# Kernel tuning notes

Measured on AMD Instinct MI355X. Metric: run time of the kernel, lower is better.

Reference implementation:

```python
import jax, jax.numpy as jnp
import numpy as np

N = 8192          # number of samples (atoms)
D_IN = 256        # in_features (descriptor dim)
D_OUT = 256       # out_features
NUM_TYPE = 64     # number of atom types
INIT_VAL = 0.01


def setup_inputs() -> dict:
    key = jax.random.key(0)
    k1, k2, k3, k4 = jax.random.split(key, 4)
    batch_i = jax.random.randint(k1, (N,), 0, NUM_TYPE)                     # [N] type index per sample
    batch_descriptor = jax.random.normal(k2, (N, D_IN), dtype=jnp.float32)  # [N, D_IN]
    layer1 = INIT_VAL * jax.random.normal(k3, (NUM_TYPE, D_OUT, D_IN), dtype=jnp.float32)
    W = INIT_VAL * jax.random.normal(k4, (D_OUT, D_IN), dtype=jnp.float32)  # linear_adjust.weight
    b = jnp.zeros((D_OUT,), dtype=jnp.float32)                              # linear_adjust.bias (init 0)
    return {"batch_i": batch_i, "batch_descriptor": batch_descriptor,
            "layer1": layer1, "W": W, "b": b}


def reference(batch_i, batch_descriptor, layer1, W, b):
    # Per-sample type-indexed weight gather + batched mat-vec (torch.bmm)
    # layer1[batch_i]: [N, D_OUT, D_IN]; descriptor: [N, D_IN] -> [N, D_OUT]
    gathered = layer1[batch_i]
    out = jnp.einsum('noi,ni->no', gathered, batch_descriptor)
    out = jnp.tanh(out)  # ACT assumed tanh (undefined in snippet)
    # linear_adjust: x @ W.T + b
    adjust = batch_descriptor @ W.T + b
    return out + adjust
```

## Files before the change

### kernel.cpp

```cpp
#include <hip/hip_runtime.h>
#include <cstddef>

#define NUM_TYPE 64
#define DD 256
#define NN 8192
#define PSTR 264
#define PT 512

typedef __bf16 bf16x8 __attribute__((ext_vector_type(8)));
typedef __bf16 bf16x4 __attribute__((ext_vector_type(4)));
typedef float f32x4 __attribute__((ext_vector_type(4)));

__device__ __forceinline__ bf16x4 cvt4(float4 v) {
  bf16x4 h;
  h[0] = (__bf16)v.x; h[1] = (__bf16)v.y; h[2] = (__bf16)v.z; h[3] = (__bf16)v.w;
  return h;
}

__device__ __forceinline__ float tanh_fast(float x) {
  float xc = fminf(fmaxf(x, -15.f), 15.f);
  float e = __expf(2.f * xc);
  return (e - 1.f) / (e + 1.f);
}

__global__ __launch_bounds__(1024) void perm_conv(
    const int* __restrict__ bi,
    const float* __restrict__ desc,
    const float* __restrict__ W,
    int* __restrict__ type_off, int* __restrict__ perm,
    __bf16* __restrict__ descB, __bf16* __restrict__ Wb) {
  const int b = blockIdx.x;
  const int tid = threadIdx.x;
  if (b == 0) {
    __shared__ int wcnt[16][NUM_TYPE];
    __shared__ int wbase[16][NUM_TYPE];
    __shared__ int cnt[NUM_TYPE];
    __shared__ int tstart[NUM_TYPE];
    __shared__ int totals[1];
    const int w = tid >> 6;
    for (int i = tid; i < 16 * NUM_TYPE; i += 1024) ((int*)wcnt)[i] = 0;
    __syncthreads();
    int myv[8];
#pragma unroll
    for (int rnd = 0; rnd < 8; ++rnd) {
      int v = bi[rnd * 1024 + tid];
      myv[rnd] = v;
      atomicAdd(&wcnt[w][v], 1);
    }
    __syncthreads();
    if (tid < NUM_TYPE) {
      int s = 0;
#pragma unroll
      for (int ww = 0; ww < 16; ++ww) { wbase[ww][tid] = s; s += wcnt[ww][tid]; }
      cnt[tid] = s;
    }
    __syncthreads();
    if (tid == 0) {
      int s = 0;
      for (int t = 0; t < NUM_TYPE; ++t) { tstart[t] = s; s += cnt[t]; }
      totals[0] = s;
    }
    __syncthreads();
    if (tid < NUM_TYPE) {
      const int s0 = tstart[tid];
      type_off[tid] = s0;
#pragma unroll
      for (int ww = 0; ww < 16; ++ww) wbase[ww][tid] += s0;
    }
    if (tid == 0) type_off[NUM_TYPE] = totals[0];
    __syncthreads();
#pragma unroll
    for (int rnd = 0; rnd < 8; ++rnd) {
      int v = myv[rnd];
      int p = atomicAdd(&wbase[w][v], 1);
      perm[p] = rnd * 1024 + tid;
    }
  } else {
    const float4* srcD = reinterpret_cast<const float4*>(desc);
    const float4* srcW = reinterpret_cast<const float4*>(W);
#pragma unroll
    for (int it = 0; it < 2; ++it) {
      const int idx = (b - 1) * 2048 + it * 1024 + tid;
      if (idx < 524288)
        *reinterpret_cast<bf16x4*>(descB + (size_t)idx * 4) = cvt4(srcD[idx]);
      else
        *reinterpret_cast<bf16x4*>(Wb + (size_t)(idx - 524288) * 4) = cvt4(srcW[idx - 524288]);
    }
  }
}

__global__ __launch_bounds__(512, 2) void gemm_res32(
    const __bf16* __restrict__ descB,
    const float* __restrict__ layer1,
    const __bf16* __restrict__ Wb,
    const float* __restrict__ bias,
    const int* __restrict__ type_off,
    const int* __restrict__ perm,
    float* __restrict__ out) {
  extern __shared__ __bf16 lds[];
  __bf16* At = lds;
  __bf16* Ll = lds + 64 * DD;
  __bf16* Wl = Ll + 32 * PSTR;
  int* ptile = (int*)(Wl + 32 * PSTR);

  const int d = blockIdx.x;
  const int t = (d & 7) + 8 * ((d >> 3) & 7);
  const int cb = d >> 6;
  const int off = type_off[t];
  const int limit = type_off[t + 1];
  const int cnt = limit - off;
  if (cnt <= 0) return;
  const int ngr = (cnt + 63) >> 6;

  const int tid = threadIdx.x;
  const int wid = tid >> 6;
  const int lane = tid & 63;
  const int l15 = lane & 15;
  const int lg = lane >> 4;
  const int wr = wid >> 1;
  const int wc = wid & 1;

  for (int i = tid; i < cnt && i < PT; i += 512) ptile[i] = perm[off + i];

  {
    const float* Lsrc = layer1 + ((size_t)t * DD + cb * 32) * DD;
#pragma unroll
    for (int it = 0; it < 4; ++it) {
      const int idx = it * 512 + tid;
      const int col = idx >> 6, seg = idx & 63;
      *reinterpret_cast<bf16x4*>(Ll + col * PSTR + seg * 4) =
          cvt4(*reinterpret_cast<const float4*>(Lsrc + (size_t)col * DD + seg * 4));
    }
    const __bf16* Wsrc = Wb + (size_t)(cb * 32) * DD;
#pragma unroll
    for (int it = 0; it < 2; ++it) {
      const int idx = it * 512 + tid;
      const int col = idx >> 5, seg = idx & 31;
      *reinterpret_cast<bf16x8*>(Wl + col * PSTR + seg * 8) =
          *reinterpret_cast<const bf16x8*>(Wsrc + (size_t)col * DD + seg * 8);
    }
  }
  __syncthreads();

  const int colg = cb * 32 + wc * 16 + l15;
  const float bv = bias[colg];

#define A_ISSUE(firstLocal)                                                   \
  {                                                                           \
    _Pragma("unroll")                                                         \
    for (int it = 0; it < 4; ++it) {                                          \
      const int r0 = wid * 8 + it * 2;                                        \
      const int row = r0 + (lane >> 5);                                       \
      int lr = (firstLocal) + row;                                            \
      if (lr >= cnt) lr = cnt - 1;                                            \
      const int pv = (lr < PT) ? ptile[lr] : perm[off + lr];                  \
      const int segg = (lane & 31) ^ (row & 7);                               \
      const __bf16* gsrc = descB + (size_t)pv * DD + segg * 8;                \
      __builtin_amdgcn_global_load_lds(                                       \
          (const __attribute__((address_space(1))) void*)gsrc,                \
          (__attribute__((address_space(3))) void*)(At + r0 * DD),            \
          16, 0, 0);                                                          \
    }                                                                         \
  }

  A_ISSUE(0)
  asm volatile("s_waitcnt vmcnt(0)" ::: "memory");
  __syncthreads();

  for (int j = 0; j < ngr; ++j) {
    const int rowA = wr * 16 + l15;
    const int rsw = rowA & 7;
    f32x4 accL = {0.f, 0.f, 0.f, 0.f};
    f32x4 accW = {0.f, 0.f, 0.f, 0.f};
#pragma unroll
    for (int kc = 0; kc < 8; ++kc) {
      const int c0 = (kc * 4 + lg) ^ rsw;
      bf16x8 af = *reinterpret_cast<const bf16x8*>(At + rowA * DD + c0 * 8);
      bf16x8 bl = *reinterpret_cast<const bf16x8*>(Ll + (wc * 16 + l15) * PSTR + kc * 32 + lg * 8);
      bf16x8 bw = *reinterpret_cast<const bf16x8*>(Wl + (wc * 16 + l15) * PSTR + kc * 32 + lg * 8);
      accL = __builtin_amdgcn_mfma_f32_16x16x32_bf16(af, bl, accL, 0, 0, 0);
      accW = __builtin_amdgcn_mfma_f32_16x16x32_bf16(af, bw, accW, 0, 0, 0);
    }

    const int olr = j * 64 + rowA;
    int sOut = -1;
    if (olr < cnt) sOut = (olr < PT) ? ptile[olr] : perm[off + olr];
#pragma unroll
    for (int i = 0; i < 4; ++i) {
      const int sv = __shfl(sOut, lg * 4 + i, 64);
      if (sv >= 0)
        __builtin_nontemporal_store(tanh_fast(accL[i]) + accW[i] + bv,
                                    out + (size_t)sv * DD + colg);
    }

    if (j + 1 < ngr) {
      __syncthreads();
      A_ISSUE((j + 1) * 64)
      asm volatile("s_waitcnt vmcnt(0)" ::: "memory");
      __syncthreads();
    }
  }
#undef A_ISSUE
}

extern "C" void kernel_launch(void* const* d_in, const int* in_sizes, int n_in,
                              void* d_out, int out_size, void* d_ws, size_t ws_size,
                              hipStream_t stream) {
  const int* bi       = (const int*)d_in[0];
  const float* desc   = (const float*)d_in[1];
  const float* layer1 = (const float*)d_in[2];
  const float* W      = (const float*)d_in[3];
  const float* bias   = (const float*)d_in[4];
  float* out = (float*)d_out;

  char* ws = (char*)d_ws;
  int* type_off = (int*)(ws);
  int* perm     = (int*)(ws + 8192);
  __bf16* descB = (__bf16*)(ws + 65536);
  __bf16* Wb    = (__bf16*)(ws + 65536 + 4194304);

  const int ldsBytes = 64 * DD * 2 + 2 * 32 * PSTR * 2 + PT * 4;

  hipLaunchKernelGGL(perm_conv, dim3(265), dim3(1024), 0, stream,
                     bi, desc, W, type_off, perm, descB, Wb);
  hipLaunchKernelGGL(gemm_res32, dim3(512), dim3(512), ldsBytes, stream,
                     descB, layer1, Wb, bias, type_off, perm, out);
}
```

Baseline: 23.83 us.

## Double-buffer gathered descriptor tiles and keep W fragments in registers

Adds a second LDS buffer for the gathered descriptor rows, so the next 64-row group is prefetched with global_load_lds while the current group is multiplied. Instead of waiting for every load, the kernel waits with vmcnt(4) so the prefetch can stay in flight. The W operand now lives in registers (Wf[8]) rather than LDS, and the layer1 tile uses an XOR swizzle in place of padding. The LDS perm cache is dropped in favour of direct global reads of perm. This hides gather latency and removes W LDS reads, at the cost of more VGPRs, which may reduce occupancy under launch_bounds(512,2), plus extra global perm loads.

Result: slower. 25.17 us (+5.6%).

```diff
diff --git a/kernel.cpp b/kernel.cpp
--- a/kernel.cpp
+++ b/kernel.cpp
@@ -4,8 +4,6 @@
 #define NUM_TYPE 64
 #define DD 256
 #define NN 8192
-#define PSTR 264
-#define PT 512
 
 typedef __bf16 bf16x8 __attribute__((ext_vector_type(8)));
 typedef __bf16 bf16x4 __attribute__((ext_vector_type(4)));
@@ -98,10 +96,9 @@
     const int* __restrict__ perm,
     float* __restrict__ out) {
   extern __shared__ __bf16 lds[];
-  __bf16* At = lds;
-  __bf16* Ll = lds + 64 * DD;
-  __bf16* Wl = Ll + 32 * PSTR;
-  int* ptile = (int*)(Wl + 32 * PSTR);
+  __bf16* At0 = lds;
+  __bf16* At1 = lds + 64 * DD;
+  __bf16* Ll  = lds + 128 * DD;
 
   const int d = blockIdx.x;
   const int t = (d & 7) + 8 * ((d >> 3) & 7);
@@ -119,33 +116,27 @@
   const int lg = lane >> 4;
   const int wr = wid >> 1;
   const int wc = wid & 1;
-
-  for (int i = tid; i < cnt && i < PT; i += 512) ptile[i] = perm[off + i];
+  const int colg = cb * 32 + wc * 16 + l15;
+
+  bf16x8 Wf[8];
+#pragma unroll
+  for (int kc = 0; kc < 8; ++kc)
+    Wf[kc] = *reinterpret_cast<const bf16x8*>(Wb + (size_t)colg * DD + kc * 32 + lg * 8);
+  const float bv = bias[colg];
 
   {
     const float* Lsrc = layer1 + ((size_t)t * DD + cb * 32) * DD;
 #pragma unroll
     for (int it = 0; it < 4; ++it) {
       const int idx = it * 512 + tid;
-      const int col = idx >> 6, seg = idx & 63;
-      *reinterpret_cast<bf16x4*>(Ll + col * PSTR + seg * 4) =
-          cvt4(*reinterpret_cast<const float4*>(Lsrc + (size_t)col * DD + seg * 4));
-    }
-    const __bf16* Wsrc = Wb + (size_t)(cb * 32) * DD;
-#pragma unroll
-    for (int it = 0; it < 2; ++it) {
-      const int idx = it * 512 + tid;
-      const int col = idx >> 5, seg = idx & 31;
-      *reinterpret_cast<bf16x8*>(Wl + col * PSTR + seg * 8) =
-          *reinterpret_cast<const bf16x8*>(Wsrc + (size_t)col * DD + seg * 8);
-    }
-  }
-  __syncthreads();
-
-  const int colg = cb * 32 + wc * 16 + l15;
-  const float bv = bias[colg];
-
-#define A_ISSUE(firstLocal)                                                   \
+      const int col = idx >> 6, s4 = idx & 63;
+      const int chunk = (s4 >> 1) ^ (col & 7);
+      *reinterpret_cast<bf16x4*>(Ll + col * DD + chunk * 8 + (s4 & 1) * 4) =
+          cvt4(*reinterpret_cast<const float4*>(Lsrc + (size_t)col * DD + s4 * 4));
+    }
+  }
+
+#define A_ISSUE(firstLocal, bp)                                               \
   {                                                                           \
     _Pragma("unroll")                                                         \
     for (int it = 0; it < 4; ++it) {                                          \
@@ -153,38 +144,47 @@
       const int row = r0 + (lane >> 5);                                       \
       int lr = (firstLocal) + row;                                            \
       if (lr >= cnt) lr = cnt - 1;                                            \
-      const int pv = (lr < PT) ? ptile[lr] : perm[off + lr];                  \
+      const int pv = perm[off + lr];                                          \
       const int segg = (lane & 31) ^ (row & 7);                               \
       const __bf16* gsrc = descB + (size_t)pv * DD + segg * 8;                \
       __builtin_amdgcn_global_load_lds(                                       \
           (const __attribute__((address_space(1))) void*)gsrc,                \
-          (__attribute__((address_space(3))) void*)(At + r0 * DD),            \
+          (__attribute__((address_space(3))) void*)((bp) + r0 * DD),          \
           16, 0, 0);                                                          \
     }                                                                         \
   }
 
-  A_ISSUE(0)
-  asm volatile("s_waitcnt vmcnt(0)" ::: "memory");
+  A_ISSUE(0, At0)
+  if (ngr > 1) {
+    A_ISSUE(64, At1)
+    asm volatile("s_waitcnt vmcnt(4)" ::: "memory");
+  } else {
+    asm volatile("s_waitcnt vmcnt(0)" ::: "memory");
+  }
   __syncthreads();
 
+  const int rowA = wr * 16 + l15;
+  const int rsw = rowA & 7;
+  const int lrow = wc * 16 + l15;
+  const int lsw = lrow & 7;
+
   for (int j = 0; j < ngr; ++j) {
-    const int rowA = wr * 16 + l15;
-    const int rsw = rowA & 7;
+    const __bf16* Ab = (j & 1) ? At1 : At0;
+
     f32x4 accL = {0.f, 0.f, 0.f, 0.f};
     f32x4 accW = {0.f, 0.f, 0.f, 0.f};
 #pragma unroll
     for (int kc = 0; kc < 8; ++kc) {
-      const int c0 = (kc * 4 + lg) ^ rsw;
-      bf16x8 af = *reinterpret_cast<const bf16x8*>(At + rowA * DD + c0 * 8);
-      bf16x8 bl = *reinterpret_cast<const bf16x8*>(Ll + (wc * 16 + l15) * PSTR + kc * 32 + lg * 8);
-      bf16x8 bw = *reinterpret_cast<const bf16x8*>(Wl + (wc * 16 + l15) * PSTR + kc * 32 + lg * 8);
+      const int ca = (kc * 4 + lg) ^ rsw;
+      const int cl = (kc * 4 + lg) ^ lsw;
+      bf16x8 af = *reinterpret_cast<const bf16x8*>(Ab + rowA * DD + ca * 8);
+      bf16x8 bl = *reinterpret_cast<const bf16x8*>(Ll + lrow * DD + cl * 8);
       accL = __builtin_amdgcn_mfma_f32_16x16x32_bf16(af, bl, accL, 0, 0, 0);
-      accW = __builtin_amdgcn_mfma_f32_16x16x32_bf16(af, bw, accW, 0, 0, 0);
+      accW = __builtin_amdgcn_mfma_f32_16x16x32_bf16(af, Wf[kc], accW, 0, 0, 0);
     }
 
     const int olr = j * 64 + rowA;
-    int sOut = -1;
-    if (olr < cnt) sOut = (olr < PT) ? ptile[olr] : perm[off + olr];
+    const int sOut = (olr < cnt) ? perm[off + olr] : -1;
 #pragma unroll
     for (int i = 0; i < 4; ++i) {
       const int sv = __shfl(sOut, lg * 4 + i, 64);
@@ -195,8 +195,13 @@
 
     if (j + 1 < ngr) {
       __syncthreads();
-      A_ISSUE((j + 1) * 64)
-      asm volatile("s_waitcnt vmcnt(0)" ::: "memory");
+      if (j + 2 < ngr) {
+        __bf16* Anext = (j & 1) ? At1 : At0;
+        A_ISSUE((j + 2) * 64, Anext)
+        asm volatile("s_waitcnt vmcnt(4)" ::: "memory");
+      } else {
+        asm volatile("s_waitcnt vmcnt(0)" ::: "memory");
+      }
       __syncthreads();
     }
   }
@@ -219,7 +224,7 @@
   __bf16* descB = (__bf16*)(ws + 65536);
   __bf16* Wb    = (__bf16*)(ws + 65536 + 4194304);
 
-  const int ldsBytes = 64 * DD * 2 + 2 * 32 * PSTR * 2 + PT * 4;
+  const int ldsBytes = 128 * DD * 2 + 32 * DD * 2;
 
   hipLaunchKernelGGL(perm_conv, dim3(265), dim3(1024), 0, stream,
                      bi, desc, W, type_off, perm, descB, Wb);
```
